# Performance work log

Hardware: AMD Instinct MI355X
Metric: run time of the kernel (lower is better)

Reference implementation:

```python
import jax, jax.numpy as jnp
import numpy as np

# dims: B jets, K routed slots per jet, S particles, D embed, E experts, H heads
B, K, S, D, E, H = 512, 2, 128, 128, 4, 8
F = 4 * D  # ffn_dim
MAXN = 1.0 - 1e-5  # Poincare ball (c=1) max norm for projx


def _n(x):
    return jnp.sqrt(jnp.clip(jnp.sum(x * x, axis=-1, keepdims=True), 1e-15))


def expmap0(u):
    n = _n(u)
    return jnp.tanh(n) * u / n


def logmap0(x):
    n = _n(x)
    return jnp.arctanh(jnp.minimum(n, MAXN)) * x / n


def projx(x):
    n = _n(x)
    return jnp.where(n > MAXN, x * (MAXN / n), x)


def mobius_add(x, y):
    xy = jnp.sum(x * y, axis=-1, keepdims=True)
    x2 = jnp.sum(x * x, axis=-1, keepdims=True)
    y2 = jnp.sum(y * y, axis=-1, keepdims=True)
    num = (1.0 + 2.0 * xy + y2) * x + (1.0 - x2) * y
    den = 1.0 + 2.0 * xy + x2 * y2
    return num / jnp.clip(den, 1e-15)


def layernorm(x, g, b):
    m = jnp.mean(x, axis=-1, keepdims=True)
    v = jnp.mean((x - m) ** 2, axis=-1, keepdims=True)
    return g * (x - m) / jnp.sqrt(v + 1e-5) + b


def man_linear(x, W, b):
    # Manifold_Linear: mobius matvec == expmap0(W @ logmap0(x)), then mobius bias, projx
    return projx(mobius_add(expmap0(logmap0(x) @ W.T), expmap0(b)))


def mob_relu(x):
    # Mob_Act(ReLU): expmap0(relu(logmap0(x)))
    return expmap0(jax.nn.relu(logmap0(x)))


def setup_inputs():
    key = jax.random.key(0)
    ks = jax.random.split(key, 16)
    features = expmap0(0.05 * jax.random.normal(ks[0], (B, K, S, D), jnp.float32))
    # K distinct expert ids per sample (original .nonzero().item() assumes uniqueness)
    expert_indices = jnp.argsort(jax.random.uniform(ks[1], (B, E)), axis=1)[:, :K].astype(jnp.int32)
    pm = jax.random.uniform(ks[2], (B, S)) < 0.2
    pm = pm.at[:, 0].set(False)  # keep at least one valid token per row
    w = lambda k, shp, sc: sc * jax.random.normal(k, shp, jnp.float32)
    s = 1.0 / np.sqrt(D)
    sf = 1.0 / np.sqrt(F)
    return dict(
        features=features, expert_indices=expert_indices, padding_mask=pm,
        ln1_g=jnp.ones((E, D)), ln1_b=jnp.zeros((E, D)),
        ln2_g=jnp.ones((E, D)), ln2_b=jnp.zeros((E, D)),
        wq=w(ks[3], (E, D, D), s), bq=w(ks[4], (E, D), 0.02),
        wk=w(ks[5], (E, D, D), s), bk=w(ks[6], (E, D), 0.02),
        wv=w(ks[7], (E, D, D), s), bv=w(ks[8], (E, D), 0.02),
        wo=w(ks[9], (E, D, D), s), bo=w(ks[10], (E, D), 0.02),
        fc1_w=w(ks[11], (E, F, D), s), fc1_b=w(ks[12], (E, F), 0.02),
        fc2_w=w(ks[13], (E, D, F), sf), fc2_b=w(ks[14], (E, D), 0.02),
    )


def _mha(x, Wq, bq, Wk, bk, Wv, bv, Wo, bo, pad_bias):
    b, s, d = x.shape
    hd = d // H
    q = logmap0(man_linear(x, Wq, bq)).reshape(b, s, H, hd)
    k = logmap0(man_linear(x, Wk, bk)).reshape(b, s, H, hd)
    v = logmap0(man_linear(x, Wv, bv)).reshape(b, s, H, hd)
    scores = jnp.einsum('bqhd,bkhd->bhqk', q, k) * (1.0 / np.sqrt(hd)) + pad_bias
    att = jax.nn.softmax(scores, axis=-1)
    ctx = jnp.einsum('bhqk,bkhd->bqhd', att, v).reshape(b, s, d)
    return man_linear(expmap0(ctx), Wo, bo)


def _expert(x, e, P, pad_bias):
    res = x
    h = expmap0(layernorm(logmap0(x), P['ln1_g'][e], P['ln1_b'][e]))
    h = projx(_mha(h, P['wq'][e], P['bq'][e], P['wk'][e], P['bk'][e],
                   P['wv'][e], P['bv'][e], P['wo'][e], P['bo'][e], pad_bias))
    x = projx(mobius_add(h, res))
    res = x
    h = projx(expmap0(layernorm(logmap0(x), P['ln2_g'][e], P['ln2_b'][e])))
    h = projx(mob_relu(man_linear(h, P['fc1_w'][e], P['fc1_b'][e])))
    h = mob_relu(man_linear(h, P['fc2_w'][e], P['fc2_b'][e]))
    return projx(mobius_add(h, res))


def reference(features, expert_indices, padding_mask,
              ln1_g, ln1_b, ln2_g, ln2_b,
              wq, bq, wk, bk, wv, bv, wo, bo,
              fc1_w, fc1_b, fc2_w, fc2_b):
    P = dict(ln1_g=ln1_g, ln1_b=ln1_b, ln2_g=ln2_g, ln2_b=ln2_b,
             wq=wq, bq=bq, wk=wk, bk=bk, wv=wv, bv=bv, wo=wo, bo=bo,
             fc1_w=fc1_w, fc1_b=fc1_b, fc2_w=fc2_w, fc2_b=fc2_b)
    pad_bias = jnp.where(padding_mask, -1e9, 0.0)[:, None, None, :]  # [B,1,1,S]
    outs = []
    for e in range(E):  # small fixed expert loop (distinct params)
        sel = expert_indices == e  # [B,K]
        present = jnp.any(sel, axis=1)  # [B]
        slot = jnp.argmax(sel, axis=1)  # [B]
        x = jnp.take_along_axis(features, slot[:, None, None, None], axis=1)[:, 0]  # [B,S,D]
        y = _expert(x, e, P, pad_bias)
        outs.append(jnp.where(present[:, None, None], y, 0.0))
    return jnp.stack(outs, axis=1)  # [B,E,S,D]; zero rows where expert not routed
```

## Files before the change

kernel.cpp:

```cpp
#include <hip/hip_runtime.h>
#include <stdint.h>

#define SS 128
#define DD 128
#define EE 4
#define HH 8
#define HDIM 16
#define FF 512
#define BB 512
#define KK 2
#define NTASK (BB*KK)
#define MAXNF 0.99999f
#define NW3 786432

typedef unsigned short u16;
typedef unsigned int u32;

typedef __attribute__((ext_vector_type(8))) short s8v;
typedef __attribute__((ext_vector_type(4))) float f4v;

#define MFMA32(a,b,c) __builtin_amdgcn_mfma_f32_16x16x32_bf16(a,b,c,0,0,0)

__device__ __forceinline__ float bf2f(u16 h){ return __uint_as_float(((u32)h)<<16); }
__device__ __forceinline__ u16 f2bf(float f){
  u32 x = __float_as_uint(f);
  u32 r = x + 0x7FFFu + ((x>>16)&1u);
  return (u16)(r>>16);
}
__device__ __forceinline__ float bfl(u32 u){ return __uint_as_float(u<<16); }
__device__ __forceinline__ float bfh(u32 u){ return __uint_as_float(u & 0xFFFF0000u); }

__device__ __forceinline__ float wsum(float v){
  #pragma unroll
  for(int off=32; off>0; off>>=1) v += __shfl_xor(v, off, 64);
  return v;
}
__device__ __forceinline__ float wmax(float v){
  #pragma unroll
  for(int off=32; off>0; off>>=1) v = fmaxf(v, __shfl_xor(v, off, 64));
  return v;
}
__device__ __forceinline__ float artanhf_(float x){ return 0.5f*logf((1.f+x)/(1.f-x)); }

__device__ __forceinline__ u32 cvtpk(float a, float b){
  u32 r; asm("v_cvt_pk_bf16_f32 %0, %1, %2" : "=v"(r) : "v"(a), "v"(b)); return r;
}
__device__ __forceinline__ void split2(float a, float b, u32& H, u32& M, u32& L){
  H = cvtpk(a,b);
  float ra = a - bfl(H), rb = b - bfh(H);
  M = cvtpk(ra,rb);
  float sa = ra - bfl(M), sb = rb - bfh(M);
  L = cvtpk(sa,sb);
}
__device__ __forceinline__ void split8(const float* v, s8v& H, s8v& M, s8v& L){
  union { u32 w[4]; s8v s; } uh, um, ul;
  #pragma unroll
  for(int p=0;p<4;++p){
    u32 a,bq2,c; split2(v[2*p], v[2*p+1], a, bq2, c);
    uh.w[p]=a; um.w[p]=bq2; ul.w[p]=c;
  }
  H=uh.s; M=um.s; L=ul.s;
}
__device__ __forceinline__ s8v sel8(int c, s8v a, s8v b){ return c ? a : b; }

__device__ __forceinline__ u32 xf32(int row, int colf){
  return (u32)row*512u + (((u32)colf*4u) ^ (((u32)row&7u)<<4));
}
__device__ __forceinline__ u32 xfr_(int row, int colf){
  return (u32)row*2048u + (((u32)colf*4u) ^ (((u32)row&7u)<<4));
}

__device__ __forceinline__ void mkA512(const char* T, int row, int colf, int hm, s8v& A1, s8v& A2){
  float va[8];
  float4 v0 = *(const float4*)(T + xf32(row, colf));
// ... 68 lines not shown
  #pragma unroll
  for(int i=0;i<NPL;++i) v[i]*=sc;
}
template<int NPL> __device__ __forceinline__ void f_projx(float* v){
  float n = vnorm<NPL>(v);
  if(n > MAXNF){
    float sc = MAXNF/n;
    #pragma unroll
    for(int i=0;i<NPL;++i) v[i]*=sc;
  }
}
template<int NPL> __device__ __forceinline__ void f_mobius_add(float* x, const float* y){
  float xy=0.f, x2=0.f, y2=0.f;
  #pragma unroll
  for(int i=0;i<NPL;++i){ xy+=x[i]*y[i]; x2+=x[i]*x[i]; y2+=y[i]*y[i]; }
  xy=wsum(xy); x2=wsum(x2); y2=wsum(y2);
  float cx = 1.f + 2.f*xy + y2;
  float cy = 1.f - x2;
  float den = fmaxf(1.f + 2.f*xy + x2*y2, 1e-15f);
  float inv = 1.f/den;
  #pragma unroll
  for(int i=0;i<NPL;++i) x[i] = (cx*x[i] + cy*y[i])*inv;
}
template<int NPL> __device__ __forceinline__ void f_layernorm(float* v, const float* g, const float* b){
  const float invD = 1.f/(float)(NPL*64);
  float m=0.f;
  #pragma unroll
  for(int i=0;i<NPL;++i) m += v[i];
  m = wsum(m)*invD;
  float s2=0.f;
  #pragma unroll
  for(int i=0;i<NPL;++i){ v[i]-=m; s2 += v[i]*v[i]; }
  s2 = wsum(s2)*invD;
  float inv = 1.f/sqrtf(s2+1e-5f);
  #pragma unroll
  for(int i=0;i<NPL;++i) v[i] = g[i]*(v[i]*inv) + b[i];
}

__global__ void prep_kernel(const u16* __restrict__ feat16,
                            const unsigned char* __restrict__ mask,
                            float* __restrict__ mbias, int* __restrict__ flag){
  __shared__ int s_stats, s_max, s_nan;
  if(threadIdx.x==0){ s_stats=0; s_max=0; s_nan=0; }
  __syncthreads();
  int c=0;
  for(int i=threadIdx.x; i<131072; i+=blockDim.x){
    u16 v = feat16[i];
    if(((v>>7)&0xFFu)==0xFFu) c++;
  }
  if(c) atomicAdd(&s_nan, c);
  int lstats=0, lmax=0;
  for(int i=threadIdx.x; i<BB*SS; i+=blockDim.x){
    int v = mask[i];
    if(v){
      lmax = v>lmax ? v : lmax;
      if((i&3)==1) lstats|=1;
      if((i&3)!=0) lstats|=2;
    }
  }
  if(lstats) atomicOr(&s_stats, lstats);
  atomicMax(&s_max, lmax);
  __syncthreads();
  if(threadIdx.x==0) *flag = (s_nan>0) ? 1 : 0;
  int mode;
  if(s_max<=1) mode = (s_stats&2) ? 0 : 1;
  else         mode = (s_stats&1) ? 2 : 3;
// ... 30 lines not shown
  int i = blockIdx.x*256 + threadIdx.x;
  if(i >= NW3) return;
  float x;
  if(i < 65536)       x = wq[i];
  else if(i < 131072) x = wk[i-65536];
  else if(i < 196608) x = wv[i-131072];
  else if(i < 262144) x = wo[i-196608];
  else if(i < 524288) x = f1w[i-262144];
  else                x = f2w[i-524288];
  u32 H,M,L; split2(x,x,H,M,L);
  wsp[i]         = (u16)H;
  wsp[NW3 + i]   = (u16)M;
  wsp[2*NW3 + i] = (u16)L;
}

__global__ __launch_bounds__(512)
void moe_f32(const int* __restrict__ flag,
             const float* __restrict__ feat, const int* __restrict__ eidx,
             const float* __restrict__ mbias,
             const float* __restrict__ ln1g, const float* __restrict__ ln1b,
             const float* __restrict__ ln2g, const float* __restrict__ ln2b,
             const float* __restrict__ bq, const float* __restrict__ bk_,
             const float* __restrict__ bv, const float* __restrict__ bo,
             const float* __restrict__ f1b, const float* __restrict__ f2b,
             const u16* __restrict__ wsp,
             float* __restrict__ out, int ntask)
{
  if(*flag != 1) return;

  __shared__ __align__(16) char LB[163840];
  char* UF  = LB;
  char* R2  = LB + 65536;
  char* SX  = LB + 131072;
  char* VTS = LB + 131072 + 16384;

  const int tid = threadIdx.x;
  const int lane = tid & 63;
  const int w    = tid >> 6;
  const int ll   = lane & 15;
  const int hl   = lane >> 4;
  const int hm   = (hl < 2);

  for(int task = blockIdx.x; task < ntask; task += gridDim.x){
    __syncthreads();
    const int b = task >> 1, slot = task & 1;
    const int e  = eidx[b*KK + slot];
    const int eo = eidx[b*KK + (slot^1)];
    int used = (1<<e)|(1<<eo), sp = 0, cnt = 0;
    #pragma unroll
    for(int t2=0;t2<4;++t2){ if(!((used>>t2)&1)){ if(cnt==slot) sp=t2; cnt++; } }
    const float* X = feat + (size_t)task * (SS*DD);
    float* own   = out + ((size_t)(b*EE+e )) * (SS*DD);
    float* spare = out + ((size_t)(b*EE+sp)) * (SS*DD);

    float g1[2],b1[2],g2[2],b2[2],ebq[2],ebk[2],ebv[2],ebo[2],ebf2[2],ebf1[8];
    {
      float2 t0;
      t0 = *(const float2*)(ln1g + e*DD + 2*lane); g1[0]=t0.x; g1[1]=t0.y;
      t0 = *(const float2*)(ln1b + e*DD + 2*lane); b1[0]=t0.x; b1[1]=t0.y;
      t0 = *(const float2*)(ln2g + e*DD + 2*lane); g2[0]=t0.x; g2[1]=t0.y;
      t0 = *(const float2*)(ln2b + e*DD + 2*lane); b2[0]=t0.x; b2[1]=t0.y;
      t0 = *(const float2*)(bq  + e*DD + 2*lane); ebq[0]=t0.x; ebq[1]=t0.y; f_expmap0<2>(ebq);
      t0 = *(const float2*)(bk_ + e*DD + 2*lane); ebk[0]=t0.x; ebk[1]=t0.y; f_expmap0<2>(ebk);
      t0 = *(const float2*)(bv  + e*DD + 2*lane); ebv[0]=t0.x; ebv[1]=t0.y; f_expmap0<2>(ebv);
      t0 = *(const float2*)(bo  + e*DD + 2*lane); ebo[0]=t0.x; ebo[1]=t0.y; f_expmap0<2>(ebo);
      t0 = *(const float2*)(f2b + e*DD + 2*lane); ebf2[0]=t0.x; ebf2[1]=t0.y; f_expmap0<2>(ebf2);
      #pragma unroll
      for(int j2=0;j2<4;++j2){
        t0 = *(const float2*)(f1b + e*FF + 2*lane + 128*j2); ebf1[2*j2]=t0.x; ebf1[2*j2+1]=t0.y;
      }
      f_expmap0<8>(ebf1);
    }
    float mb_reg[8];
    #pragma unroll
    for(int nt=0;nt<8;++nt) mb_reg[nt] = mbias[b*SS + nt*16 + ll];

    for(int r=0;r<16;++r){
      int t = w*16 + r;
      float2 xv = *(const float2*)(X + t*DD + 2*lane);
      float v[2] = {xv.x, xv.y};
      f_logmap0<2>(v);
      f_layernorm<2>(v, g1, b1);
      f_expmap0<2>(v);
      f_logmap0<2>(v);
      float2 o2; o2.x=v[0]; o2.y=v[1];
      *(float2*)(UF + xf32(t, 2*lane)) = o2;
    }
    __syncthreads();

    #pragma unroll
    for(int m=0;m<3;++m){
      const u32 tb = (u32)m*65536u + (u32)e*16384u;
      s8v Bh[8], Blm[8];
      {
        int nrow = w*16 + ll;
        #pragma unroll
        for(int c=0;c<8;++c){
          u32 koff = c*16 + (hl&1)*8;
          Bh[c]  = *(const s8v*)(wsp + tb + nrow*128 + koff);
          Blm[c] = *(const s8v*)(wsp + (hm?2:1)*NW3 + tb + nrow*128 + koff);
        }
      }
      for(int ch=0; ch<4; ++ch){
        #pragma unroll
        for(int sub=0; sub<2; ++sub){
          int arow = (2*ch+sub)*16 + ll;
          s8v A1v[8], A2v[8];
          #pragma unroll
          for(int c=0;c<8;++c)
            mkA512(UF, arow, c*16 + (hl&1)*8, hm, A1v[c], A2v[c]);
          f4v acc = {0.f,0.f,0.f,0.f};
          #pragma unroll
          for(int c=0;c<8;++c){
            s8v B3 = sel8(hm, Bh[c], Blm[c]);
            acc = MFMA32(A1v[c], Bh[c], acc);
            acc = MFMA32(A1v[c], Blm[c], acc);
            acc = MFMA32(A2v[c], B3, acc);
          }
          #pragma unroll
          for(int i=0;i<4;++i)
            *(float*)(SX + xf32(sub*16 + hl*4 + i, w*16 + ll)) = acc[i];
        }
        __syncthreads();
        for(int rr=0; rr<4; ++rr){
          int lr = w*4 + rr; int t = ch*32 + lr;
          float2 pp = *(const float2*)(SX + xf32(lr, 2*lane));
          float v[2] = {pp.x, pp.y};
          f_expmap0<2>(v);
          float eb[2];
          if(m==0){ eb[0]=ebq[0]; eb[1]=ebq[1]; }
          else if(m==1){ eb[0]=ebk[0]; eb[1]=ebk[1]; }
          else { eb[0]=ebv[0]; eb[1]=ebv[1]; }
          f_mobius_add<2>(v, eb);
          f_projx<2>(v);
          f_logmap0<2>(v);
          if(m==0){
            float2 o2; o2.x=v[0]; o2.y=v[1];
            *(float2*)(spare + t*DD + 2*lane) = o2;
          } else if(m==1){
            float2 o2; o2.x=v[0]; o2.y=v[1];
            *(float2*)(R2 + xf32(t, 2*lane)) = o2;
          } else {
            *(float*)(VTS + (2*lane)*128   + lr*4) = v[0];
            *(float*)(VTS + (2*lane+1)*128 + lr*4) = v[1];
          }
        }
        __syncthreads();
        if(m==2){
          int d = tid >> 2, kk = (tid & 3) * 8;
          float4 a0 = *(const float4*)(VTS + d*128 + kk*4);
          float4 a1 = *(const float4*)(VTS + d*128 + kk*4 + 16);
          *(float4*)(own + (size_t)d*DD + ch*32 + kk)     = a0;
          *(float4*)(own + (size_t)d*DD + ch*32 + kk + 4) = a1;
        }
      }
    }
    __syncthreads();

    for(int h=0; h<HH; ++h){
      {
        int tok = tid & 127, dq = tid >> 7;
        float4 vv = *(const float4*)(R2 + xf32(tok, h*16 + dq*4));
        u32 H0,M0,L0,H1,M1,L1;
        split2(vv.x,vv.y,H0,M0,L0); split2(vv.z,vv.w,H1,M1,L1);
        u32 o = (u32)tok*48u + (u32)dq*8u;
        *(u32*)(SX + 0*6144 + o) = H0; *(u32*)(SX + 0*6144 + o + 4) = H1;
        *(u32*)(SX + 1*6144 + o) = M0; *(u32*)(SX + 1*6144 + o + 4) = M1;
        *(u32*)(SX + 2*6144 + o) = L0; *(u32*)(SX + 2*6144 + o + 4) = L1;
      }
      __syncthreads();
      float qa[8];
      {
        float4 q0 = *(const float4*)(spare + (w*16+ll)*DD + h*16 + (hl&1)*8);
        float4 q1 = *(const float4*)(spare + (w*16+ll)*DD + h*16 + (hl&1)*8 + 4);
        qa[0]=q0.x; qa[1]=q0.y; qa[2]=q0.z; qa[3]=q0.w;
        qa[4]=q1.x; qa[5]=q1.y; qa[6]=q1.z; qa[7]=q1.w;
      }
      s8v QH,QM,QL; split8(qa, QH,QM,QL);
      s8v qA1 = sel8(hm, QH, QM);
      s8v qA2 = sel8(hm, QL, QH);
      f4v sc[8];
      #pragma unroll
      for(int nt=0;nt<8;++nt){
        u32 o = (u32)(nt*16+ll)*48u + (u32)(hl&1)*16u;
        s8v B1 = *(const s8v*)(SX + 0*6144 + o);
        s8v B2 = *(const s8v*)(SX + (hm?2:1)*6144 + o);
        s8v B3 = sel8(hm, B1, B2);
        f4v z = {0.f,0.f,0.f,0.f};
        z = MFMA32(qA1, B1, z);
        z = MFMA32(qA1, B2, z);
        z = MFMA32(qA2, B3, z);
        sc[nt] = z;
      }
      __syncthreads();
      #pragma unroll
      for(int i=0;i<4;++i){
        float p8[8]; float mx = -3e38f;
        #pragma unroll
        for(int nt=0;nt<8;++nt){ p8[nt] = sc[nt][i]*0.25f + mb_reg[nt]; mx = fmaxf(mx, p8[nt]); }
        #pragma unroll
        for(int o=1;o<16;o<<=1) mx = fmaxf(mx, __shfl_xor(mx, o, 64));
        float dn = 0.f;
        #pragma unroll
        for(int nt=0;nt<8;++nt){ p8[nt] = expf(p8[nt]-mx); dn += p8[nt]; }
        #pragma unroll
        for(int o=1;o<16;o<<=1) dn += __shfl_xor(dn, o, 64);
        float inv = 1.f/dn;
        #pragma unroll
        for(int nt=0;nt<8;++nt)
          *(float*)(UF + xf32(w*16 + hl*4 + i, nt*16 + ll)) = p8[nt]*inv;
      }
      f4v ca = {0.f,0.f,0.f,0.f};
      #pragma unroll
      for(int c=0;c<8;++c){
        float pa[8];
        {
          float4 p0 = *(const float4*)(UF + xf32(w*16+ll, c*16 + (hl&1)*8));
          float4 p1 = *(const float4*)(UF + xf32(w*16+ll, c*16 + (hl&1)*8 + 4));
          pa[0]=p0.x; pa[1]=p0.y; pa[2]=p0.z; pa[3]=p0.w;
          pa[4]=p1.x; pa[5]=p1.y; pa[6]=p1.z; pa[7]=p1.w;
        }
        s8v PH,PM,PL; split8(pa, PH,PM,PL);
        s8v pA1 = sel8(hm, PH, PM);
        s8v pA2 = sel8(hm, PL, PH);
        float va[8];
        {
          const float* vp = own + (h*16+ll)*DD + c*16 + (hl&1)*8;
          float4 v0 = *(const float4*)(vp);
          float4 v1 = *(const float4*)(vp + 4);
          va[0]=v0.x; va[1]=v0.y; va[2]=v0.z; va[3]=v0.w;
          va[4]=v1.x; va[5]=v1.y; va[6]=v1.z; va[7]=v1.w;
        }
        s8v VH,VM,VL; split8(va, VH,VM,VL);
        s8v vB2 = sel8(hm, VL, VM);
        s8v vB3 = sel8(hm, VH, VM);
        ca = MFMA32(pA1, VH, ca);
        ca = MFMA32(pA1, vB2, ca);
        ca = MFMA32(pA2, vB3, ca);
      }
      #pragma unroll
      for(int i=0;i<4;++i)
        *(float*)(R2 + xf32(w*16 + hl*4 + i, h*16 + ll)) = ca[i];
    }
    __syncthreads();

    for(int r=0;r<16;++r){
      int t = w*16 + r;
      float2 cc2 = *(const float2*)(R2 + xf32(t, 2*lane));
      float v[2] = {cc2.x, cc2.y};
      f_expmap0<2>(v);
      f_logmap0<2>(v);
      float2 o2; o2.x=v[0]; o2.y=v[1];
      *(float2*)(UF + xf32(t, 2*lane)) = o2;
    }
    __syncthreads();

    {
      const u32 tb = 196608u + (u32)e*16384u;
      s8v Bh[8], Blm[8];
      {
        int nrow = w*16 + ll;
        #pragma unroll
        for(int c=0;c<8;++c){
          u32 koff = c*16 + (hl&1)*8;
          Bh[c]  = *(const s8v*)(wsp + tb + nrow*128 + koff);
          Blm[c] = *(const s8v*)(wsp + (hm?2:1)*NW3 + tb + nrow*128 + koff);
        }
      }
      for(int ch=0; ch<4; ++ch){
        #pragma unroll
        for(int sub=0; sub<2; ++sub){
          int arow = (2*ch+sub)*16 + ll;
          s8v A1v[8], A2v[8];
          #pragma unroll
          for(int c=0;c<8;++c)
            mkA512(UF, arow, c*16 + (hl&1)*8, hm, A1v[c], A2v[c]);
          f4v acc = {0.f,0.f,0.f,0.f};
          #pragma unroll
          for(int c=0;c<8;++c){
            s8v B3 = sel8(hm, Bh[c], Blm[c]);
            acc = MFMA32(A1v[c], Bh[c], acc);
            acc = MFMA32(A1v[c], Blm[c], acc);
            acc = MFMA32(A2v[c], B3, acc);
          }
          #pragma unroll
          for(int i=0;i<4;++i)
            *(float*)(SX + xf32(sub*16 + hl*4 + i, w*16 + ll)) = acc[i];
        }
        __syncthreads();
        for(int rr=0; rr<4; ++rr){
          int lr = w*4 + rr; int t = ch*32 + lr;
          float2 pp = *(const float2*)(SX + xf32(lr, 2*lane));
          float v[2] = {pp.x, pp.y};
          f_expmap0<2>(v);
          f_mobius_add<2>(v, ebo);
          f_projx<2>(v);
          f_projx<2>(v);
          float2 rr2 = *(const float2*)(X + t*DD + 2*lane);
          float res[2] = {rr2.x, rr2.y};
          f_mobius_add<2>(v, res);
          f_projx<2>(v);
          float2 xo; xo.x=v[0]; xo.y=v[1];
          *(float2*)(own + t*DD + 2*lane) = xo;
          f_logmap0<2>(v);
          f_layernorm<2>(v, g2, b2);
          f_expmap0<2>(v);
          f_projx<2>(v);
          f_logmap0<2>(v);
          float2 o2; o2.x=v[0]; o2.y=v[1];
          *(float2*)(UF + xf32(t, 2*lane)) = o2;
        }
        __syncthreads();
      }
    }

    for(int tc=0; tc<4; ++tc){
      const int t0 = tc*32;
      {
        #pragma unroll
        for(int mt=0; mt<2; ++mt){
          int arow = t0 + mt*16 + ll;
          s8v A1v[8], A2v[8];
          #pragma unroll
          for(int c=0;c<8;++c)
            mkA512(UF, arow, c*16 + (hl&1)*8, hm, A1v[c], A2v[c]);
          #pragma unroll
          for(int n4=0;n4<4;++n4){
            u32 nrow = (u32)(w*64 + n4*16 + ll);
            f4v acc = {0.f,0.f,0.f,0.f};
            #pragma unroll
            for(int c=0;c<8;++c){
              u32 koff = c*16 + (hl&1)*8;
              s8v B1 = *(const s8v*)(wsp + 262144u + (u32)e*65536u + nrow*128 + koff);
              s8v B2 = *(const s8v*)(wsp + (hm?2:1)*NW3 + 262144u + (u32)e*65536u + nrow*128 + koff);
              s8v B3 = sel8(hm, B1, B2);
              acc = MFMA32(A1v[c], B1, acc);
              acc = MFMA32(A1v[c], B2, acc);
              acc = MFMA32(A2v[c], B3, acc);
            }
            #pragma unroll
            for(int i=0;i<4;++i)
              *(float*)(R2 + xfr_(mt*16 + hl*4 + i, w*64 + n4*16 + ll)) = acc[i];
          }
        }
      }
      __syncthreads();
      for(int rr=0; rr<4; ++rr){
        int lr = w*4 + rr;
        float v[8];
        #pragma unroll
        for(int j2=0;j2<4;++j2){
          float2 pp = *(const float2*)(R2 + xfr_(lr, 2*lane + 128*j2));
          v[2*j2]=pp.x; v[2*j2+1]=pp.y;
        }
        f_expmap0<8>(v);
        f_mobius_add<8>(v, ebf1);
        f_projx<8>(v);
        f_logmap0<8>(v);
        #pragma unroll
        for(int i=0;i<8;++i) v[i] = fmaxf(v[i], 0.f);
        f_expmap0<8>(v);
        f_projx<8>(v);
        f_logmap0<8>(v);
        #pragma unroll
        for(int j2=0;j2<4;++j2){
          float2 o2; o2.x=v[2*j2]; o2.y=v[2*j2+1];
          *(float2*)(R2 + xfr_(lr, 2*lane + 128*j2)) = o2;
        }
      }
      __syncthreads();
      {
        u32 nrow = (u32)(w*16 + ll);
        #pragma unroll
        for(int mt=0; mt<2; ++mt){
          f4v ga = {0.f,0.f,0.f,0.f};
          #pragma unroll
          for(int grp=0; grp<4; ++grp){
            s8v A1v[8], A2v[8];
            #pragma unroll
            for(int cc=0;cc<8;++cc)
              mkA2048(R2, mt*16 + ll, (grp*8+cc)*16 + (hl&1)*8, hm, A1v[cc], A2v[cc]);
            #pragma unroll
            for(int cc=0;cc<8;++cc){
              int c = grp*8 + cc;
              u32 koff = c*16 + (hl&1)*8;
              s8v B1 = *(const s8v*)(wsp + 524288u + (u32)e*65536u + nrow*512 + koff);
              s8v B2 = *(const s8v*)(wsp + (hm?2:1)*NW3 + 524288u + (u32)e*65536u + nrow*512 + koff);
              s8v B3 = sel8(hm, B1, B2);
              ga = MFMA32(A1v[cc], B1, ga);
              ga = MFMA32(A1v[cc], B2, ga);
              ga = MFMA32(A2v[cc], B3, ga);
            }
          }
          #pragma unroll
          for(int i=0;i<4;++i)
            *(float*)(SX + xf32(mt*16 + hl*4 + i, w*16 + ll)) = ga[i];
        }
      }
      __syncthreads();
      for(int rr=0; rr<4; ++rr){
        int lr = w*4 + rr; int gt = t0 + lr;
        float v[2];
        v[0] = *(const float*)(SX + xf32(lr, 2*lane));
        v[1] = *(const float*)(SX + xf32(lr, 2*lane+1));
        f_expmap0<2>(v);
        f_mobius_add<2>(v, ebf2);
        f_projx<2>(v);
        f_logmap0<2>(v);
        v[0]=fmaxf(v[0],0.f); v[1]=fmaxf(v[1],0.f);
        f_expmap0<2>(v);
        float2 xx = *(const float2*)(own + gt*DD + 2*lane);
        float x1v[2] = {xx.x, xx.y};
        f_mobius_add<2>(v, x1v);
        f_projx<2>(v);
        float2 o2; o2.x=v[0]; o2.y=v[1];
        *(float2*)(own + gt*DD + 2*lane) = o2;
      }
      __syncthreads();
    }

    {
      float4 z4 = {0.f,0.f,0.f,0.f};
      for(int i=tid; i<4096; i+=512) *(float4*)(spare + 4*i) = z4;
    }
  }
}

template<typename T>
__global__ __launch_bounds__(256)
void moe_kernel(const int* __restrict__ flag,
                const T* __restrict__ feat, const int* __restrict__ eidx,
                const float* __restrict__ mbias,
                const T* __restrict__ ln1g, const T* __restrict__ ln1b,
                const T* __restrict__ ln2g, const T* __restrict__ ln2b,
                const T* __restrict__ wq, const T* __restrict__ bq,
                const T* __restrict__ wk, const T* __restrict__ bk_,
                const T* __restrict__ wv, const T* __restrict__ bv,
                const T* __restrict__ wo, const T* __restrict__ bo,
                const T* __restrict__ f1w, const T* __restrict__ f1b,
                const T* __restrict__ f2w, const T* __restrict__ f2b,
                T* __restrict__ out, float* __restrict__ ws, int ntask)
{
  const int want = (sizeof(T)==4) ? 1 : 0;
  if(*flag != want) return;

  __shared__ float U[SS*DD];
  const int tid  = threadIdx.x;
  const int lane = tid & 63;
  const int wid  = tid >> 6;
  float* T0 = ws + (size_t)blockIdx.x * (4*SS*DD);
  float* T1 = T0 + SS*DD;
// ... 262 lines not shown
```

Before: 3.682 ms.

## Compute QKV and out-projection epilogues in MFMA registers, dropping LDS staging and barriers

Each wave now computes a full 16-row by 128-column tile of the QKV and output projections, keeping all eight accumulators in registers. The hyperbolic epilogue (expmap, mobius add, projx, logmap, layernorm) then runs directly on the MFMA fragment layout, using 16-lane shuffle reductions instead of round-tripping through LDS. This removes the per-chunk LDS staging, the V transpose buffer and many __syncthreads. In exchange, weights are no longer held in registers across chunks and are reloaded from global memory per tile. V is stored untransposed and read with strided global loads in the attention step. Register pressure also rises with eight accumulators live.

```diff
diff --git a/kernel.cpp b/kernel.cpp
--- a/kernel.cpp
+++ b/kernel.cpp
@@ -40,6 +40,11 @@
   for(int off=32; off>0; off>>=1) v = fmaxf(v, __shfl_xor(v, off, 64));
   return v;
 }
+__device__ __forceinline__ float rsum16(float v){
+  #pragma unroll
+  for(int off=8; off>0; off>>=1) v += __shfl_xor(v, off, 64);
+  return v;
+}
 __device__ __forceinline__ float artanhf_(float x){ return 0.5f*logf((1.f+x)/(1.f-x)); }
 
 __device__ __forceinline__ u32 cvtpk(float a, float b){
@@ -174,6 +179,60 @@
   #pragma unroll
   for(int i=0;i<NPL;++i){ v[i]-=m; s2 += v[i]*v[i]; }
   s2 = wsum(s2)*invD;
+  float inv = 1.f/sqrtf(s2+1e-5f);
+  #pragma unroll
+  for(int i=0;i<NPL;++i) v[i] = g[i]*(v[i]*inv) + b[i];
+}
+
+template<int NPL> __device__ __forceinline__ float vnorm16(const float* v){
+  float s=0.f;
+  #pragma unroll
+  for(int i=0;i<NPL;++i) s += v[i]*v[i];
+  s = rsum16(s);
+  return sqrtf(fmaxf(s, 1e-15f));
+}
+template<int NPL> __device__ __forceinline__ void f16_logmap0(float* v){
+  float n = vnorm16<NPL>(v);
+  float sc = artanhf_(fminf(n, MAXNF))/n;
+  #pragma unroll
+  for(int i=0;i<NPL;++i) v[i]*=sc;
+}
+template<int NPL> __device__ __forceinline__ void f16_expmap0(float* v){
+  float n = vnorm16<NPL>(v);
+  float sc = tanhf(n)/n;
+  #pragma unroll
+  for(int i=0;i<NPL;++i) v[i]*=sc;
+}
+template<int NPL> __device__ __forceinline__ void f16_projx(float* v){
+  float n = vnorm16<NPL>(v);
+  if(n > MAXNF){
+    float sc = MAXNF/n;
+    #pragma unroll
+    for(int i=0;i<NPL;++i) v[i]*=sc;
+  }
+}
+template<int NPL> __device__ __forceinline__ void f16_mobius_add(float* x, const float* y){
+  float xy=0.f, x2=0.f, y2=0.f;
+  #pragma unroll
+  for(int i=0;i<NPL;++i){ xy+=x[i]*y[i]; x2+=x[i]*x[i]; y2+=y[i]*y[i]; }
+  xy=rsum16(xy); x2=rsum16(x2); y2=rsum16(y2);
+  float cx = 1.f + 2.f*xy + y2;
+  float cy = 1.f - x2;
+  float den = fmaxf(1.f + 2.f*xy + x2*y2, 1e-15f);
+  float inv = 1.f/den;
+  #pragma unroll
+  for(int i=0;i<NPL;++i) x[i] = (cx*x[i] + cy*y[i])*inv;
+}
+template<int NPL> __device__ __forceinline__ void f16_layernorm(float* v, const float* g, const float* b){
+  const float invD = 1.f/(float)(NPL*16);
+  float m=0.f;
+  #pragma unroll
+  for(int i=0;i<NPL;++i) m += v[i];
+  m = rsum16(m)*invD;
+  float s2=0.f;
+  #pragma unroll
+  for(int i=0;i<NPL;++i){ v[i]-=m; s2 += v[i]*v[i]; }
+  s2 = rsum16(s2)*invD;
   float inv = 1.f/sqrtf(s2+1e-5f);
   #pragma unroll
   for(int i=0;i<NPL;++i) v[i] = g[i]*(v[i]*inv) + b[i];
@@ -270,7 +329,6 @@
   char* UF  = LB;
   char* R2  = LB + 65536;
   char* SX  = LB + 131072;
-  char* VTS = LB + 131072 + 16384;
 
   const int tid = threadIdx.x;
   const int lane = tid & 63;
@@ -291,194 +349,176 @@
     float* own   = out + ((size_t)(b*EE+e )) * (SS*DD);
     float* spare = out + ((size_t)(b*EE+sp)) * (SS*DD);
 
-    float g1[2],b1[2],g2[2],b2[2],ebq[2],ebk[2],ebv[2],ebo[2],ebf2[2],ebf1[8];
     {
+      float g1[2],b1[2];
       float2 t0;
       t0 = *(const float2*)(ln1g + e*DD + 2*lane); g1[0]=t0.x; g1[1]=t0.y;
       t0 = *(const float2*)(ln1b + e*DD + 2*lane); b1[0]=t0.x; b1[1]=t0.y;
-      t0 = *(const float2*)(ln2g + e*DD + 2*lane); g2[0]=t0.x; g2[1]=t0.y;
-      t0 = *(const float2*)(ln2b + e*DD + 2*lane); b2[0]=t0.x; b2[1]=t0.y;
-      t0 = *(const float2*)(bq  + e*DD + 2*lane); ebq[0]=t0.x; ebq[1]=t0.y; f_expmap0<2>(ebq);
-      t0 = *(const float2*)(bk_ + e*DD + 2*lane); ebk[0]=t0.x; ebk[1]=t0.y; f_expmap0<2>(ebk);
-      t0 = *(const float2*)(bv  + e*DD + 2*lane); ebv[0]=t0.x; ebv[1]=t0.y; f_expmap0<2>(ebv);
-      t0 = *(const float2*)(bo  + e*DD + 2*lane); ebo[0]=t0.x; ebo[1]=t0.y; f_expmap0<2>(ebo);
-      t0 = *(const float2*)(f2b + e*DD + 2*lane); ebf2[0]=t0.x; ebf2[1]=t0.y; f_expmap0<2>(ebf2);
+      for(int r=0;r<16;++r){
+        int t = w*16 + r;
+        float2 xv = *(const float2*)(X + t*DD + 2*lane);
+        float v[2] = {xv.x, xv.y};
+        f_logmap0<2>(v);
+        f_layernorm<2>(v, g1, b1);
+        f_expmap0<2>(v);
+        f_logmap0<2>(v);
+        float2 o2; o2.x=v[0]; o2.y=v[1];
+        *(float2*)(UF + xf32(t, 2*lane)) = o2;
+      }
+    }
+    __syncthreads();
+
+    {
+      float ebq8[8], ebk8[8], ebv8[8];
       #pragma unroll
-      for(int j2=0;j2<4;++j2){
-        t0 = *(const float2*)(f1b + e*FF + 2*lane + 128*j2); ebf1[2*j2]=t0.x; ebf1[2*j2+1]=t0.y;
-      }
-      f_expmap0<8>(ebf1);
-    }
-    float mb_reg[8];
-    #pragma unroll
-    for(int nt=0;nt<8;++nt) mb_reg[nt] = mbias[b*SS + nt*16 + ll];
-
-    for(int r=0;r<16;++r){
-      int t = w*16 + r;
-      float2 xv = *(const float2*)(X + t*DD + 2*lane);
-      float v[2] = {xv.x, xv.y};
-      f_logmap0<2>(v);
-      f_layernorm<2>(v, g1, b1);
-      f_expmap0<2>(v);
-      f_logmap0<2>(v);
-      float2 o2; o2.x=v[0]; o2.y=v[1];
-      *(float2*)(UF + xf32(t, 2*lane)) = o2;
-    }
-    __syncthreads();
-
-    #pragma unroll
-    for(int m=0;m<3;++m){
-      const u32 tb = (u32)m*65536u + (u32)e*16384u;
-      s8v Bh[8], Blm[8];
-      {
-        int nrow = w*16 + ll;
+      for(int n=0;n<8;++n){
+        ebq8[n] = bq [e*DD + n*16 + ll];
+        ebk8[n] = bk_[e*DD + n*16 + ll];
+        ebv8[n] = bv [e*DD + n*16 + ll];
+      }
+      f16_expmap0<8>(ebq8); f16_expmap0<8>(ebk8); f16_expmap0<8>(ebv8);
+
+      #pragma unroll
+      for(int m=0;m<3;++m){
+        const u32 tb = (u32)m*65536u + (u32)e*16384u;
+        s8v A1v[8], A2v[8];
+        #pragma unroll
+        for(int c=0;c<8;++c)
+          mkA512(UF, w*16+ll, c*16 + (hl&1)*8, hm, A1v[c], A2v[c]);
+        f4v acc[8];
+        #pragma unroll
+        for(int n=0;n<8;++n){ acc[n][0]=0.f; acc[n][1]=0.f; acc[n][2]=0.f; acc[n][3]=0.f; }
+        #pragma unroll
+        for(int n=0;n<8;++n){
+          u32 nrow = (u32)(n*16 + ll);
+          #pragma unroll
+          for(int c=0;c<8;++c){
+            u32 koff = c*16 + (hl&1)*8;
+            s8v B1 = *(const s8v*)(wsp + tb + nrow*128 + koff);
+            s8v B2 = *(const s8v*)(wsp + (hm?2:1)*NW3 + tb + nrow*128 + koff);
+            s8v B3 = sel8(hm, B1, B2);
+            acc[n] = MFMA32(A1v[c], B1, acc[n]);
+            acc[n] = MFMA32(A1v[c], B2, acc[n]);
+            acc[n] = MFMA32(A2v[c], B3, acc[n]);
+          }
+        }
+        #pragma unroll
+        for(int i=0;i<4;++i){
+          int r = w*16 + hl*4 + i;
+          float v[8];
+          #pragma unroll
+          for(int n=0;n<8;++n) v[n] = acc[n][i];
+          f16_expmap0<8>(v);
+          float eb[8];
+          #pragma unroll
+          for(int n=0;n<8;++n) eb[n] = (m==0) ? ebq8[n] : (m==1) ? ebk8[n] : ebv8[n];
+          f16_mobius_add<8>(v, eb);
+          f16_projx<8>(v);
+          f16_logmap0<8>(v);
+          if(m==0){
+            #pragma unroll
+            for(int n=0;n<8;++n) spare[(size_t)r*DD + n*16 + ll] = v[n];
+          } else if(m==1){
+            #pragma unroll
+            for(int n=0;n<8;++n) *(float*)(R2 + xf32(r, n*16 + ll)) = v[n];
+          } else {
+            #pragma unroll
+            for(int n=0;n<8;++n) own[(size_t)r*DD + n*16 + ll] = v[n];
+          }
+        }
+      }
+    }
+    __syncthreads();
+
+    {
+      float mb_reg[8];
+      #pragma unroll
+      for(int nt=0;nt<8;++nt) mb_reg[nt] = mbias[b*SS + nt*16 + ll];
+
+      for(int h=0; h<HH; ++h){
+        {
+          int tok = tid & 127, dq = tid >> 7;
+          float4 vv = *(const float4*)(R2 + xf32(tok, h*16 + dq*4));
+          u32 H0,M0,L0,H1,M1,L1;
+          split2(vv.x,vv.y,H0,M0,L0); split2(vv.z,vv.w,H1,M1,L1);
+          u32 o = (u32)tok*48u + (u32)dq*8u;
+          *(u32*)(SX + 0*6144 + o) = H0; *(u32*)(SX + 0*6144 + o + 4) = H1;
+          *(u32*)(SX + 1*6144 + o) = M0; *(u32*)(SX + 1*6144 + o + 4) = M1;
+          *(u32*)(SX + 2*6144 + o) = L0; *(u32*)(SX + 2*6144 + o + 4) = L1;
+        }
+        __syncthreads();
+        float qa[8];
+        {
+          float4 q0 = *(const float4*)(spare + (w*16+ll)*DD + h*16 + (hl&1)*8);
+          float4 q1 = *(const float4*)(spare + (w*16+ll)*DD + h*16 + (hl&1)*8 + 4);
+          qa[0]=q0.x; qa[1]=q0.y; qa[2]=q0.z; qa[3]=q0.w;
+          qa[4]=q1.x; qa[5]=q1.y; qa[6]=q1.z; qa[7]=q1.w;
+        }
+        s8v QH,QM,QL; split8(qa, QH,QM,QL);
+        s8v qA1 = sel8(hm, QH, QM);
+        s8v qA2 = sel8(hm, QL, QH);
+        f4v sc[8];
+        #pragma unroll
+        for(int nt=0;nt<8;++nt){
+          u32 o = (u32)(nt*16+ll)*48u + (u32)(hl&1)*16u;
+          s8v B1 = *(const s8v*)(SX + 0*6144 + o);
+          s8v B2 = *(const s8v*)(SX + (hm?2:1)*6144 + o);
+          s8v B3 = sel8(hm, B1, B2);
+          f4v z = {0.f,0.f,0.f,0.f};
+          z = MFMA32(qA1, B1, z);
+          z = MFMA32(qA1, B2, z);
+          z = MFMA32(qA2, B3, z);
+          sc[nt] = z;
+        }
+        __syncthreads();
+        #pragma unroll
+        for(int i=0;i<4;++i){
+          float p8[8]; float mx = -3e38f;
+          #pragma unroll
+          for(int nt=0;nt<8;++nt){ p8[nt] = sc[nt][i]*0.25f + mb_reg[nt]; mx = fmaxf(mx, p8[nt]); }
+          #pragma unroll
+          for(int o=1;o<16;o<<=1) mx = fmaxf(mx, __shfl_xor(mx, o, 64));
+          float dn = 0.f;
+          #pragma unroll
+          for(int nt=0;nt<8;++nt){ p8[nt] = expf(p8[nt]-mx); dn += p8[nt]; }
+          #pragma unroll
+          for(int o=1;o<16;o<<=1) dn += __shfl_xor(dn, o, 64);
+          float inv = 1.f/dn;
+          #pragma unroll
+          for(int nt=0;nt<8;++nt)
+            *(float*)(UF + xf32(w*16 + hl*4 + i, nt*16 + ll)) = p8[nt]*inv;
+        }
+        f4v ca = {0.f,0.f,0.f,0.f};
         #pragma unroll
         for(int c=0;c<8;++c){
-          u32 koff = c*16 + (hl&1)*8;
-          Bh[c]  = *(const s8v*)(wsp + tb + nrow*128 + koff);
-          Blm[c] = *(const s8v*)(wsp + (hm?2:1)*NW3 + tb + nrow*128 + koff);
-        }
-      }
-      for(int ch=0; ch<4; ++ch){
-        #pragma unroll
-        for(int sub=0; sub<2; ++sub){
-          int arow = (2*ch+sub)*16 + ll;
-          s8v A1v[8], A2v[8];
-          #pragma unroll
-          for(int c=0;c<8;++c)
-            mkA512(UF, arow, c*16 + (hl&1)*8, hm, A1v[c], A2v[c]);
-          f4v acc = {0.f,0.f,0.f,0.f};
-          #pragma unroll
-          for(int c=0;c<8;++c){
-            s8v B3 = sel8(hm, Bh[c], Blm[c]);
-            acc = MFMA32(A1v[c], Bh[c], acc);
-            acc = MFMA32(A1v[c], Blm[c], acc);
-            acc = MFMA32(A2v[c], B3, acc);
-          }
-          #pragma unroll
-          for(int i=0;i<4;++i)
-            *(float*)(SX + xf32(sub*16 + hl*4 + i, w*16 + ll)) = acc[i];
-        }
-        __syncthreads();
-        for(int rr=0; rr<4; ++rr){
-          int lr = w*4 + rr; int t = ch*32 + lr;
-          float2 pp = *(const float2*)(SX + xf32(lr, 2*lane));
-          float v[2] = {pp.x, pp.y};
-          f_expmap0<2>(v);
-          float eb[2];
-          if(m==0){ eb[0]=ebq[0]; eb[1]=ebq[1]; }
-          else if(m==1){ eb[0]=ebk[0]; eb[1]=ebk[1]; }
-          else { eb[0]=ebv[0]; eb[1]=ebv[1]; }
-          f_mobius_add<2>(v, eb);
-          f_projx<2>(v);
-          f_logmap0<2>(v);
-          if(m==0){
-            float2 o2; o2.x=v[0]; o2.y=v[1];
-            *(float2*)(spare + t*DD + 2*lane) = o2;
-          } else if(m==1){
-            float2 o2; o2.x=v[0]; o2.y=v[1];
-            *(float2*)(R2 + xf32(t, 2*lane)) = o2;
-          } else {
-            *(float*)(VTS + (2*lane)*128   + lr*4) = v[0];
-            *(float*)(VTS + (2*lane+1)*128 + lr*4) = v[1];
-          }
-        }
-        __syncthreads();
-        if(m==2){
-          int d = tid >> 2, kk = (tid & 3) * 8;
-          float4 a0 = *(const float4*)(VTS + d*128 + kk*4);
-          float4 a1 = *(const float4*)(VTS + d*128 + kk*4 + 16);
-          *(float4*)(own + (size_t)d*DD + ch*32 + kk)     = a0;
-          *(float4*)(own + (size_t)d*DD + ch*32 + kk + 4) = a1;
-        }
-      }
-    }
-    __syncthreads();
-
-    for(int h=0; h<HH; ++h){
-      {
-        int tok = tid & 127, dq = tid >> 7;
-        float4 vv = *(const float4*)(R2 + xf32(tok, h*16 + dq*4));
-        u32 H0,M0,L0,H1,M1,L1;
-        split2(vv.x,vv.y,H0,M0,L0); split2(vv.z,vv.w,H1,M1,L1);
-        u32 o = (u32)tok*48u + (u32)dq*8u;
-        *(u32*)(SX + 0*6144 + o) = H0; *(u32*)(SX + 0*6144 + o + 4) = H1;
-        *(u32*)(SX + 1*6144 + o) = M0; *(u32*)(SX + 1*6144 + o + 4) = M1;
-        *(u32*)(SX + 2*6144 + o) = L0; *(u32*)(SX + 2*6144 + o + 4) = L1;
-      }
-      __syncthreads();
-      float qa[8];
-      {
-        float4 q0 = *(const float4*)(spare + (w*16+ll)*DD + h*16 + (hl&1)*8);
-        float4 q1 = *(const float4*)(spare + (w*16+ll)*DD + h*16 + (hl&1)*8 + 4);
-        qa[0]=q0.x; qa[1]=q0.y; qa[2]=q0.z; qa[3]=q0.w;
-        qa[4]=q1.x; qa[5]=q1.y; qa[6]=q1.z; qa[7]=q1.w;
-      }
-      s8v QH,QM,QL; split8(qa, QH,QM,QL);
-      s8v qA1 = sel8(hm, QH, QM);
-      s8v qA2 = sel8(hm, QL, QH);
-      f4v sc[8];
-      #pragma unroll
-      for(int nt=0;nt<8;++nt){
-        u32 o = (u32)(nt*16+ll)*48u + (u32)(hl&1)*16u;
-        s8v B1 = *(const s8v*)(SX + 0*6144 + o);
-        s8v B2 = *(const s8v*)(SX + (hm?2:1)*6144 + o);
-        s8v B3 = sel8(hm, B1, B2);
-        f4v z = {0.f,0.f,0.f,0.f};
-        z = MFMA32(qA1, B1, z);
-        z = MFMA32(qA1, B2, z);
-        z = MFMA32(qA2, B3, z);
-        sc[nt] = z;
-      }
-      __syncthreads();
-      #pragma unroll
-      for(int i=0;i<4;++i){
-        float p8[8]; float mx = -3e38f;
-        #pragma unroll
-        for(int nt=0;nt<8;++nt){ p8[nt] = sc[nt][i]*0.25f + mb_reg[nt]; mx = fmaxf(mx, p8[nt]); }
-        #pragma unroll
-        for(int o=1;o<16;o<<=1) mx = fmaxf(mx, __shfl_xor(mx, o, 64));
-        float dn = 0.f;
-        #pragma unroll
-        for(int nt=0;nt<8;++nt){ p8[nt] = expf(p8[nt]-mx); dn += p8[nt]; }
-        #pragma unroll
-        for(int o=1;o<16;o<<=1) dn += __shfl_xor(dn, o, 64);
-        float inv = 1.f/dn;
-        #pragma unroll
-        for(int nt=0;nt<8;++nt)
-          *(float*)(UF + xf32(w*16 + hl*4 + i, nt*16 + ll)) = p8[nt]*inv;
-      }
-      f4v ca = {0.f,0.f,0.f,0.f};
-      #pragma unroll
-      for(int c=0;c<8;++c){
-        float pa[8];
-        {
-          float4 p0 = *(const float4*)(UF + xf32(w*16+ll, c*16 + (hl&1)*8));
-          float4 p1 = *(const float4*)(UF + xf32(w*16+ll, c*16 + (hl&1)*8 + 4));
-          pa[0]=p0.x; pa[1]=p0.y; pa[2]=p0.z; pa[3]=p0.w;
-          pa[4]=p1.x; pa[5]=p1.y; pa[6]=p1.z; pa[7]=p1.w;
-        }
-        s8v PH,PM,PL; split8(pa, PH,PM,PL);
-        s8v pA1 = sel8(hm, PH, PM);
-        s8v pA2 = sel8(hm, PL, PH);
-        float va[8];
-        {
-          const float* vp = own + (h*16+ll)*DD + c*16 + (hl&1)*8;
-          float4 v0 = *(const float4*)(vp);
-          float4 v1 = *(const float4*)(vp + 4);
-          va[0]=v0.x; va[1]=v0.y; va[2]=v0.z; va[3]=v0.w;
-          va[4]=v1.x; va[5]=v1.y; va[6]=v1.z; va[7]=v1.w;
-        }
-        s8v VH,VM,VL; split8(va, VH,VM,VL);
-        s8v vB2 = sel8(hm, VL, VM);
-        s8v vB3 = sel8(hm, VH, VM);
-        ca = MFMA32(pA1, VH, ca);
-        ca = MFMA32(pA1, vB2, ca);
-        ca = MFMA32(pA2, vB3, ca);
-      }
-      #pragma unroll
-      for(int i=0;i<4;++i)
-        *(float*)(R2 + xf32(w*16 + hl*4 + i, h*16 + ll)) = ca[i];
+          float pa[8];
+          {
+            float4 p0 = *(const float4*)(UF + xf32(w*16+ll, c*16 + (hl&1)*8));
+            float4 p1 = *(const float4*)(UF + xf32(w*16+ll, c*16 + (hl&1)*8 + 4));
+            pa[0]=p0.x; pa[1]=p0.y; pa[2]=p0.z; pa[3]=p0.w;
+            pa[4]=p1.x; pa[5]=p1.y; pa[6]=p1.z; pa[7]=p1.w;
+          }
+          s8v PH,PM,PL; split8(pa, PH,PM,PL);
+          s8v pA1 = sel8(hm, PH, PM);
+          s8v pA2 = sel8(hm, PL, PH);
+          float va[8];
+          {
+            int kbase = c*16 + (hl&1)*8;
+            #pragma unroll
+            for(int j=0;j<8;++j)
+              va[j] = own[(size_t)(kbase+j)*DD + h*16 + ll];
+          }
+          s8v VH,VM,VL; split8(va, VH,VM,VL);
+          s8v vB2 = sel8(hm, VL, VM);
+          s8v vB3 = sel8(hm, VH, VM);
+          ca = MFMA32(pA1, VH, ca);
+          ca = MFMA32(pA1, vB2, ca);
+          ca = MFMA32(pA2, vB3, ca);
+        }
+        #pragma unroll
+        for(int i=0;i<4;++i)
+          *(float*)(R2 + xf32(w*16 + hl*4 + i, h*16 + ll)) = ca[i];
+      }
     }
     __syncthreads();
 
@@ -491,170 +531,182 @@
       float2 o2; o2.x=v[0]; o2.y=v[1];
       *(float2*)(UF + xf32(t, 2*lane)) = o2;
     }
-    __syncthreads();
 
     {
+      float ebo8[8], g28[8], b28[8];
+      #pragma unroll
+      for(int n=0;n<8;++n){
+        ebo8[n] = bo  [e*DD + n*16 + ll];
+        g28[n]  = ln2g[e*DD + n*16 + ll];
+        b28[n]  = ln2b[e*DD + n*16 + ll];
+      }
+      f16_expmap0<8>(ebo8);
+
       const u32 tb = 196608u + (u32)e*16384u;
-      s8v Bh[8], Blm[8];
-      {
-        int nrow = w*16 + ll;
+      s8v A1v[8], A2v[8];
+      #pragma unroll
+      for(int c=0;c<8;++c)
+        mkA512(UF, w*16+ll, c*16 + (hl&1)*8, hm, A1v[c], A2v[c]);
+      f4v acc[8];
+      #pragma unroll
+      for(int n=0;n<8;++n){ acc[n][0]=0.f; acc[n][1]=0.f; acc[n][2]=0.f; acc[n][3]=0.f; }
+      #pragma unroll
+      for(int n=0;n<8;++n){
+        u32 nrow = (u32)(n*16 + ll);
         #pragma unroll
         for(int c=0;c<8;++c){
           u32 koff = c*16 + (hl&1)*8;
-          Bh[c]  = *(const s8v*)(wsp + tb + nrow*128 + koff);
-          Blm[c] = *(const s8v*)(wsp + (hm?2:1)*NW3 + tb + nrow*128 + koff);
-        }
-      }
-      for(int ch=0; ch<4; ++ch){
-        #pragma unroll
-        for(int sub=0; sub<2; ++sub){
-          int arow = (2*ch+sub)*16 + ll;
-          s8v A1v[8], A2v[8];
-          #pragma unroll
-          for(int c=0;c<8;++c)
-            mkA512(UF, arow, c*16 + (hl&1)*8, hm, A1v[c], A2v[c]);
-          f4v acc = {0.f,0.f,0.f,0.f};
-          #pragma unroll
-          for(int c=0;c<8;++c){
-            s8v B3 = sel8(hm, Bh[c], Blm[c]);
-            acc = MFMA32(A1v[c], Bh[c], acc);
-            acc = MFMA32(A1v[c], Blm[c], acc);
-            acc = MFMA32(A2v[c], B3, acc);
-          }
-          #pragma unroll
-          for(int i=0;i<4;++i)
-            *(float*)(SX + xf32(sub*16 + hl*4 + i, w*16 + ll)) = acc[i];
+          s8v B1 = *(const s8v*)(wsp + tb + nrow*128 + koff);
+          s8v B2 = *(const s8v*)(wsp + (hm?2:1)*NW3 + tb + nrow*128 + koff);
+          s8v B3 = sel8(hm, B1, B2);
+          acc[n] = MFMA32(A1v[c], B1, acc[n]);
+          acc[n] = MFMA32(A1v[c], B2, acc[n]);
+          acc[n] = MFMA32(A2v[c], B3, acc[n]);
+        }
+      }
+      #pragma unroll
+      for(int i=0;i<4;++i){
+        int r = w*16 + hl*4 + i;
+        float v[8];
+        #pragma unroll
+        for(int n=0;n<8;++n) v[n] = acc[n][i];
+        f16_expmap0<8>(v);
+        f16_mobius_add<8>(v, ebo8);
+        f16_projx<8>(v);
+        f16_projx<8>(v);
+        float res[8];
+        #pragma unroll
+        for(int n=0;n<8;++n) res[n] = X[(size_t)r*DD + n*16 + ll];
+        f16_mobius_add<8>(v, res);
+        f16_projx<8>(v);
+        #pragma unroll
+        for(int n=0;n<8;++n) own[(size_t)r*DD + n*16 + ll] = v[n];
+        f16_logmap0<8>(v);
+        f16_layernorm<8>(v, g28, b28);
+        f16_expmap0<8>(v);
+        f16_projx<8>(v);
+        f16_logmap0<8>(v);
+        #pragma unroll
+        for(int n=0;n<8;++n) *(float*)(UF + xf32(r, n*16 + ll)) = v[n];
+      }
+    }
+    __syncthreads();
+
+    {
+      float ebf1[8], ebf2[2];
+      {
+        float2 t0;
+        #pragma unroll
+        for(int j2=0;j2<4;++j2){
+          t0 = *(const float2*)(f1b + e*FF + 2*lane + 128*j2); ebf1[2*j2]=t0.x; ebf1[2*j2+1]=t0.y;
+        }
+        f_expmap0<8>(ebf1);
+        t0 = *(const float2*)(f2b + e*DD + 2*lane); ebf2[0]=t0.x; ebf2[1]=t0.y; f_expmap0<2>(ebf2);
+      }
+      for(int tc=0; tc<4; ++tc){
+        const int t0i = tc*32;
+        {
+          #pragma unroll
+          for(int mt=0; mt<2; ++mt){
+            int arow = t0i + mt*16 + ll;
+            s8v A1v[8], A2v[8];
+            #pragma unroll
+            for(int c=0;c<8;++c)
+              mkA512(UF, arow, c*16 + (hl&1)*8, hm, A1v[c], A2v[c]);
+            #pragma unroll
+            for(int n4=0;n4<4;++n4){
+              u32 nrow = (u32)(w*64 + n4*16 + ll);
+              f4v acc = {0.f,0.f,0.f,0.f};
+              #pragma unroll
+              for(int c=0;c<8;++c){
+                u32 koff = c*16 + (hl&1)*8;
+                s8v B1 = *(const s8v*)(wsp + 262144u + (u32)e*65536u + nrow*128 + koff);
+                s8v B2 = *(const s8v*)(wsp + (hm?2:1)*NW3 + 262144u + (u32)e*65536u + nrow*128 + koff);
+                s8v B3 = sel8(hm, B1, B2);
+                acc = MFMA32(A1v[c], B1, acc);
+                acc = MFMA32(A1v[c], B2, acc);
+                acc = MFMA32(A2v[c], B3, acc);
+              }
+              #pragma unroll
+              for(int i=0;i<4;++i)
+                *(float*)(R2 + xfr_(mt*16 + hl*4 + i, w*64 + n4*16 + ll)) = acc[i];
+            }
+          }
         }
         __syncthreads();
         for(int rr=0; rr<4; ++rr){
-          int lr = w*4 + rr; int t = ch*32 + lr;
-          float2 pp = *(const float2*)(SX + xf32(lr, 2*lane));
-          float v[2] = {pp.x, pp.y};
-          f_expmap0<2>(v);
-          f_mobius_add<2>(v, ebo);
-          f_projx<2>(v);
-          f_projx<2>(v);
-          float2 rr2 = *(const float2*)(X + t*DD + 2*lane);
-          float res[2] = {rr2.x, rr2.y};
-          f_mobius_add<2>(v, res);
-          f_projx<2>(v);
-          float2 xo; xo.x=v[0]; xo.y=v[1];
-          *(float2*)(own + t*DD + 2*lane) = xo;
-          f_logmap0<2>(v);
-          f_layernorm<2>(v, g2, b2);
-          f_expmap0<2>(v);
-          f_projx<2>(v);
-          f_logmap0<2>(v);
-          float2 o2; o2.x=v[0]; o2.y=v[1];
-          *(float2*)(UF + xf32(t, 2*lane)) = o2;
+          int lr = w*4 + rr;
+          float v[8];
+          #pragma unroll
+          for(int j2=0;j2<4;++j2){
+            float2 pp = *(const float2*)(R2 + xfr_(lr, 2*lane + 128*j2));
+            v[2*j2]=pp.x; v[2*j2+1]=pp.y;
+          }
+          f_expmap0<8>(v);
+          f_mobius_add<8>(v, ebf1);
+          f_projx<8>(v);
+          f_logmap0<8>(v);
+          #pragma unroll
+          for(int i=0;i<8;++i) v[i] = fmaxf(v[i], 0.f);
+          f_expmap0<8>(v);
+          f_projx<8>(v);
+          f_logmap0<8>(v);
+          #pragma unroll
+          for(int j2=0;j2<4;++j2){
+            float2 o2; o2.x=v[2*j2]; o2.y=v[2*j2+1];
+            *(float2*)(R2 + xfr_(lr, 2*lane + 128*j2)) = o2;
+          }
         }
         __syncthreads();
-      }
-    }
-
-    for(int tc=0; tc<4; ++tc){
-      const int t0 = tc*32;
-      {
-        #pragma unroll
-        for(int mt=0; mt<2; ++mt){
-          int arow = t0 + mt*16 + ll;
-          s8v A1v[8], A2v[8];
-          #pragma unroll
-          for(int c=0;c<8;++c)
-            mkA512(UF, arow, c*16 + (hl&1)*8, hm, A1v[c], A2v[c]);
-          #pragma unroll
-          for(int n4=0;n4<4;++n4){
-            u32 nrow = (u32)(w*64 + n4*16 + ll);
-            f4v acc = {0.f,0.f,0.f,0.f};
+        {
+          u32 nrow = (u32)(w*16 + ll);
+          #pragma unroll
+          for(int mt=0; mt<2; ++mt){
+            f4v ga = {0.f,0.f,0.f,0.f};
             #pragma unroll
-            for(int c=0;c<8;++c){
-              u32 koff = c*16 + (hl&1)*8;
-              s8v B1 = *(const s8v*)(wsp + 262144u + (u32)e*65536u + nrow*128 + koff);
-              s8v B2 = *(const s8v*)(wsp + (hm?2:1)*NW3 + 262144u + (u32)e*65536u + nrow*128 + koff);
-              s8v B3 = sel8(hm, B1, B2);
-              acc = MFMA32(A1v[c], B1, acc);
-              acc = MFMA32(A1v[c], B2, acc);
-              acc = MFMA32(A2v[c], B3, acc);
+            for(int grp=0; grp<4; ++grp){
+              s8v A1v[8], A2v[8];
+              #pragma unroll
+              for(int cc=0;cc<8;++cc)
+                mkA2048(R2, mt*16 + ll, (grp*8+cc)*16 + (hl&1)*8, hm, A1v[cc], A2v[cc]);
+              #pragma unroll
+              for(int cc=0;cc<8;++cc){
+                int c = grp*8 + cc;
+                u32 koff = c*16 + (hl&1)*8;
+                s8v B1 = *(const s8v*)(wsp + 524288u + (u32)e*65536u + nrow*512 + koff);
+                s8v B2 = *(const s8v*)(wsp + (hm?2:1)*NW3 + 524288u + (u32)e*65536u + nrow*512 + koff);
+                s8v B3 = sel8(hm, B1, B2);
+                ga = MFMA32(A1v[cc], B1, ga);
+                ga = MFMA32(A1v[cc], B2, ga);
+                ga = MFMA32(A2v[cc], B3, ga);
+              }
             }
             #pragma unroll
             for(int i=0;i<4;++i)
-              *(float*)(R2 + xfr_(mt*16 + hl*4 + i, w*64 + n4*16 + ll)) = acc[i];
-          }
-        }
-      }
-      __syncthreads();
-      for(int rr=0; rr<4; ++rr){
-        int lr = w*4 + rr;
-        float v[8];
-        #pragma unroll
-        for(int j2=0;j2<4;++j2){
-          float2 pp = *(const float2*)(R2 + xfr_(lr, 2*lane + 128*j2));
-          v[2*j2]=pp.x; v[2*j2+1]=pp.y;
-        }
-        f_expmap0<8>(v);
-        f_mobius_add<8>(v, ebf1);
-        f_projx<8>(v);
-        f_logmap0<8>(v);
-        #pragma unroll
-        for(int i=0;i<8;++i) v[i] = fmaxf(v[i], 0.f);
-        f_expmap0<8>(v);
-        f_projx<8>(v);
-        f_logmap0<8>(v);
-        #pragma unroll
-        for(int j2=0;j2<4;++j2){
-          float2 o2; o2.x=v[2*j2]; o2.y=v[2*j2+1];
-          *(float2*)(R2 + xfr_(lr, 2*lane + 128*j2)) = o2;
-        }
-      }
-      __syncthreads();
-      {
-        u32 nrow = (u32)(w*16 + ll);
-        #pragma unroll
-        for(int mt=0; mt<2; ++mt){
-          f4v ga = {0.f,0.f,0.f,0.f};
-          #pragma unroll
-          for(int grp=0; grp<4; ++grp){
-            s8v A1v[8], A2v[8];
-            #pragma unroll
-            for(int cc=0;cc<8;++cc)
-              mkA2048(R2, mt*16 + ll, (grp*8+cc)*16 + (hl&1)*8, hm, A1v[cc], A2v[cc]);
-            #pragma unroll
-            for(int cc=0;cc<8;++cc){
-              int c = grp*8 + cc;
-              u32 koff = c*16 + (hl&1)*8;
-              s8v B1 = *(const s8v*)(wsp + 524288u + (u32)e*65536u + nrow*512 + koff);
-              s8v B2 = *(const s8v*)(wsp + (hm?2:1)*NW3 + 524288u + (u32)e*65536u + nrow*512 + koff);
-              s8v B3 = sel8(hm, B1, B2);
-              ga = MFMA32(A1v[cc], B1, ga);
-              ga = MFMA32(A1v[cc], B2, ga);
-              ga = MFMA32(A2v[cc], B3, ga);
-            }
-          }
-          #pragma unroll
-          for(int i=0;i<4;++i)
-            *(float*)(SX + xf32(mt*16 + hl*4 + i, w*16 + ll)) = ga[i];
-        }
-      }
-      __syncthreads();
-      for(int rr=0; rr<4; ++rr){
-        int lr = w*4 + rr; int gt = t0 + lr;
-        float v[2];
-        v[0] = *(const float*)(SX + xf32(lr, 2*lane));
-        v[1] = *(const float*)(SX + xf32(lr, 2*lane+1));
-        f_expmap0<2>(v);
-        f_mobius_add<2>(v, ebf2);
-        f_projx<2>(v);
-        f_logmap0<2>(v);
-        v[0]=fmaxf(v[0],0.f); v[1]=fmaxf(v[1],0.f);
-        f_expmap0<2>(v);
-        float2 xx = *(const float2*)(own + gt*DD + 2*lane);
-        float x1v[2] = {xx.x, xx.y};
-        f_mobius_add<2>(v, x1v);
-        f_projx<2>(v);
-        float2 o2; o2.x=v[0]; o2.y=v[1];
-        *(float2*)(own + gt*DD + 2*lane) = o2;
-      }
-      __syncthreads();
+              *(float*)(SX + xf32(mt*16 + hl*4 + i, w*16 + ll)) = ga[i];
+          }
+        }
+        __syncthreads();
+        for(int rr=0; rr<4; ++rr){
+          int lr = w*4 + rr; int gt = t0i + lr;
+          float v[2];
+          v[0] = *(const float*)(SX + xf32(lr, 2*lane));
+          v[1] = *(const float*)(SX + xf32(lr, 2*lane+1));
+          f_expmap0<2>(v);
+          f_mobius_add<2>(v, ebf2);
+          f_projx<2>(v);
+          f_logmap0<2>(v);
+          v[0]=fmaxf(v[0],0.f); v[1]=fmaxf(v[1],0.f);
+          f_expmap0<2>(v);
+          float2 xx = *(const float2*)(own + gt*DD + 2*lane);
+          float x1v[2] = {xx.x, xx.y};
+          f_mobius_add<2>(v, x1v);
+          f_projx<2>(v);
+          float2 o2; o2.x=v[0]; o2.y=v[1];
+          *(float2*)(own + gt*DD + 2*lane) = o2;
+        }
+        __syncthreads();
+      }
     }
 
     {
```

Result: slower. 3.837 ms (+4.2%).
